# Performance work log

Measured on AMD Instinct MI355X. Metric: run time of the kernel, lower is better.

The kernel has to match this reference:

```python
import jax, jax.numpy as jnp
import numpy as np

V, F, P = 1024, 2048, 8192
_EPS = 1e-12


def setup_inputs() -> dict:
    key = jax.random.key(0)
    kv, kf, kp = jax.random.split(key, 3)
    verts = jax.random.normal(kv, (V, 3), dtype=jnp.float32)
    faces = jax.random.randint(kf, (F, 3), 0, V, dtype=jnp.int32)
    points = jax.random.normal(kp, (P, 3), dtype=jnp.float32)
    return {"verts": verts, "faces": faces, "points": points}


def _closest_point_on_tri(p, a, b, c):
    """Ericson's closest-point-on-triangle, broadcast over leading dims.
    p, a, b, c: [..., 3] -> closest point [..., 3]."""
    ab = b - a
    ac = c - a
    ap = p - a
    d1 = jnp.sum(ab * ap, -1)
    d2 = jnp.sum(ac * ap, -1)
    bp = p - b
    d3 = jnp.sum(ab * bp, -1)
    d4 = jnp.sum(ac * bp, -1)
    cp = p - c
    d5 = jnp.sum(ab * cp, -1)
    d6 = jnp.sum(ac * cp, -1)
    vc = d1 * d4 - d3 * d2
    vb = d5 * d2 - d1 * d6
    va = d3 * d6 - d5 * d4
    # guarded edge/interior parameters (denominators are >0 whenever the
    # corresponding region condition holds; eps keeps unselected branches finite)
    t_ab = d1 / jnp.maximum(d1 - d3, _EPS)
    t_ac = d2 / jnp.maximum(d2 - d6, _EPS)
    t_bc = (d4 - d3) / jnp.maximum((d4 - d3) + (d5 - d6), _EPS)
    denom = jnp.maximum(va + vb + vc, _EPS)
    v_in = vb / denom
    w_in = vc / denom
    # first-match region selection (vertex A, vertex B, edge AB, vertex C, edge AC, edge BC, interior)
    cA = (d1 <= 0) & (d2 <= 0)
    cB = (d3 >= 0) & (d4 <= d3)
    cAB = (vc <= 0) & (d1 >= 0) & (d3 <= 0)
    cC = (d6 >= 0) & (d5 <= d6)
    cAC = (vb <= 0) & (d2 >= 0) & (d6 <= 0)
    cBC = (va <= 0) & ((d4 - d3) >= 0) & ((d5 - d6) >= 0)
    z = jnp.zeros_like(d1)
    o = jnp.ones_like(d1)
    bv = jnp.select([cA, cB, cAB, cC, cAC, cBC], [z, o, t_ab, z, z, 1.0 - t_bc], v_in)
    bw = jnp.select([cA, cB, cAB, cC, cAC, cBC], [z, z, z, o, t_ac, t_bc], w_in)
    bu = 1.0 - bv - bw
    return a * bu[..., None] + b * bv[..., None] + c * bw[..., None]


def reference(verts, faces, points):
    tri = verts[faces]  # [F, 3, 3]
    a = tri[:, 0][None]  # [1, F, 3]
    b = tri[:, 1][None]
    c = tri[:, 2][None]
    cp = _closest_point_on_tri(points[:, None, :], a, b, c)  # [P, F, 3]
    dist2 = jnp.sum((points[:, None, :] - cp) ** 2, -1)  # [P, F] squared distances
    assoc = jnp.argmin(dist2, axis=1).astype(jnp.int32)  # [P] nearest triangle index
    dist = jnp.min(dist2, axis=1)  # [P]
    # loss_type == 'mse': kernel loss = sum(dist), then *= 1000 / P
    loss = jnp.sum(dist) * (1000.0 / points.shape[0])
    return loss, dist, assoc
```

## Files before the change

### kernel.cpp

```cpp
#include <hip/hip_runtime.h>

typedef float v2f __attribute__((ext_vector_type(2)));

#define P_TOTAL 8192
#define F_TOTAL 2048
#define TPB     256
#define CHUNK   256
#define NCHUNK  (F_TOTAL / CHUNK)

__device__ __forceinline__ float refine_rcp(float D) {
#pragma clang fp contract(off)
    float r0 = __builtin_amdgcn_rcpf(D);
    float e1 = __builtin_fmaf(-D, r0, 1.0f);
    return __builtin_fmaf(e1, r0, r0);
}
__device__ __forceinline__ float div_rn(float num, float D, float r) {
#pragma clang fp contract(off)
    float q0 = num * r;
    float e  = __builtin_fmaf(-D, q0, num);
    return __builtin_fmaf(e, r, q0);
}

__device__ __forceinline__ void region_select(
    float d1, float d2, float d3, float d4, float d5, float d6,
    float va, float vb, float vc, float d43, float d56,
    float g1, float g2, float g3, float g4,
    float& bu, float& bv, float& bw)
{
#pragma clang fp contract(off)
    float G1 = fmaxf(g1, 1e-12f);
    float G2 = fmaxf(g2, 1e-12f);
    float G3 = fmaxf(g3, 1e-12f);
    float G4 = fmaxf(g4, 1e-12f);

    bool cA  = (d1 <= 0.f) & (d2 <= 0.f);
    bool cB  = (d3 >= 0.f) & (d4 <= d3);
    bool cAB = (vc <= 0.f) & (d1 >= 0.f) & (d3 <= 0.f);
    bool cC  = (d6 >= 0.f) & (d5 <= d6);
    bool cAC = (vb <= 0.f) & (d2 >= 0.f) & (d6 <= 0.f);
    bool cBC = (va <= 0.f) & (d43 >= 0.f) & (d56 >= 0.f);

    float nv = cA ? 0.f : cB ? 1.f : cAB ? d1 : cC ? 0.f
             : cAC ? 0.f : cBC ? d43 : vb;
    float nw = cA ? 0.f : cB ? 0.f : cAB ? 0.f : cC ? 1.f
             : cAC ? d2 : cBC ? d43 : vc;
    float D  = cA ? 1.f : cB ? 1.f : cAB ? G1 : cC ? 1.f
             : cAC ? G2 : cBC ? G3 : G4;
    bool fBC = cBC && !(cA || cB || cAB || cC || cAC);

    float r   = refine_rcp(D);
    float qv  = div_rn(nv, D, r);
    float bww = div_rn(nw, D, r);
    float bvv = fBC ? (1.0f - qv) : qv;
    bv = bvv; bw = bww;
    bu = (1.0f - bvv) - bww;
}

__global__ __launch_bounds__(TPB) void msdf_main(
    const float* __restrict__ verts, const int* __restrict__ faces,
    const float* __restrict__ points, float* __restrict__ out)
{
#pragma clang fp contract(off)
    __shared__ float sT[9][CHUNK];
    const int tid  = threadIdx.x;
    const int lane = tid & 63;
    const int w    = tid >> 6;
    const int p    = blockIdx.x * 4 + w;

    const float px = points[3 * p], py = points[3 * p + 1], pz = points[3 * p + 2];

    unsigned int best_bits = 0xFFFFFFFFu;
    int best_idx = 0;

    for (int c = 0; c < NCHUNK; ++c) {
        __syncthreads();
        {
            int tg = c * CHUNK + tid;
            int i0 = faces[3 * tg + 0], i1 = faces[3 * tg + 1], i2 = faces[3 * tg + 2];
            sT[0][tid] = verts[3 * i0]; sT[1][tid] = verts[3 * i0 + 1]; sT[2][tid] = verts[3 * i0 + 2];
            sT[3][tid] = verts[3 * i1]; sT[4][tid] = verts[3 * i1 + 1]; sT[5][tid] = verts[3 * i1 + 2];
            sT[6][tid] = verts[3 * i2]; sT[7][tid] = verts[3 * i2 + 1]; sT[8][tid] = verts[3 * i2 + 2];
        }
        __syncthreads();

        #pragma unroll
        for (int k = 0; k < 2; ++k) {
            int base = k * 128 + 2 * lane;
            v2f ax = *(const v2f*)&sT[0][base];
            v2f ay = *(const v2f*)&sT[1][base];
            v2f az = *(const v2f*)&sT[2][base];
            v2f bx = *(const v2f*)&sT[3][base];
            v2f by = *(const v2f*)&sT[4][base];
            v2f bz = *(const v2f*)&sT[5][base];
            v2f cx = *(const v2f*)&sT[6][base];
            v2f cy = *(const v2f*)&sT[7][base];
            v2f cz = *(const v2f*)&sT[8][base];

            v2f abx = bx - ax, aby = by - ay, abz = bz - az;
            v2f acx = cx - ax, acy = cy - ay, acz = cz - az;

            v2f apx = px - ax, apy = py - ay, apz = pz - az;
            v2f d1 = (abx * apx + aby * apy) + abz * apz;
            v2f d2 = (acx * apx + acy * apy) + acz * apz;
            v2f bpx = px - bx, bpy = py - by, bpz = pz - bz;
            v2f d3 = (abx * bpx + aby * bpy) + abz * bpz;
            v2f d4 = (acx * bpx + acy * bpy) + acz * bpz;
            v2f cpx = px - cx, cpy = py - cy, cpz = pz - cz;
            v2f d5 = (abx * cpx + aby * cpy) + abz * cpz;
            v2f d6 = (acx * cpx + acy * cpy) + acz * cpz;

            v2f vc = d1 * d4 - d3 * d2;
            v2f vb = d5 * d2 - d1 * d6;
            v2f va = d3 * d6 - d5 * d4;
            v2f d43 = d4 - d3, d56 = d5 - d6;
            v2f g1 = d1 - d3;
            v2f g2 = d2 - d6;
            v2f g3 = d43 + d56;
            v2f g4 = (va + vb) + vc;

            float bu0, bv0, bw0, bu1, bv1, bw1;
            region_select(d1.x, d2.x, d3.x, d4.x, d5.x, d6.x,
                          va.x, vb.x, vc.x, d43.x, d56.x,
                          g1.x, g2.x, g3.x, g4.x, bu0, bv0, bw0);
            region_select(d1.y, d2.y, d3.y, d4.y, d5.y, d6.y,
                          va.y, vb.y, vc.y, d43.y, d56.y,
                          g1.y, g2.y, g3.y, g4.y, bu1, bv1, bw1);
            v2f bu = {bu0, bu1}, bv = {bv0, bv1}, bw = {bw0, bw1};

            v2f cpx2 = (ax * bu + bx * bv) + cx * bw;
            v2f cpy2 = (ay * bu + by * bv) + cy * bw;
            v2f cpz2 = (az * bu + bz * bv) + cz * bw;
            v2f dx = px - cpx2, dy = py - cpy2, dz = pz - cpz2;
            v2f dist2 = (dx * dx + dy * dy) + dz * dz;

            unsigned int b0 = __float_as_uint(dist2.x);
            if (b0 < best_bits) { best_bits = b0; best_idx = c * CHUNK + base; }
            unsigned int b1 = __float_as_uint(dist2.y);
            if (b1 < best_bits) { best_bits = b1; best_idx = c * CHUNK + base + 1; }
        }
    }

    unsigned long long key =
        ((unsigned long long)best_bits << 32) | (unsigned int)best_idx;
    #pragma unroll
    for (int off = 32; off > 0; off >>= 1) {
        unsigned int hi = (unsigned int)(key >> 32);
        unsigned int lo = (unsigned int)(key & 0xFFFFFFFFu);
        unsigned int ohi = __shfl_down(hi, off, 64);
        unsigned int olo = __shfl_down(lo, off, 64);
        unsigned long long ok = ((unsigned long long)ohi << 32) | olo;
        key = (ok < key) ? ok : key;
    }
    if (lane == 0) {
        out[1 + p]           = __uint_as_float((unsigned int)(key >> 32));
        out[1 + P_TOTAL + p] = (float)(unsigned int)(key & 0xFFFFFFFFu);
    }
}

__global__ __launch_bounds__(256) void msdf_loss(float* __restrict__ out)
{
    __shared__ float wsum[4];
    float s = 0.f;
    for (int k = 0; k < P_TOTAL / 256; ++k)
        s += out[1 + k * 256 + threadIdx.x];
    #pragma unroll
    for (int off = 32; off > 0; off >>= 1) s += __shfl_down(s, off, 64);
    int lane = threadIdx.x & 63, w = threadIdx.x >> 6;
    if (lane == 0) wsum[w] = s;
    __syncthreads();
    if (threadIdx.x == 0) {
        float tot = ((wsum[0] + wsum[1]) + wsum[2]) + wsum[3];
        out[0] = tot * (1000.0f / (float)P_TOTAL);
    }
}

extern "C" void kernel_launch(void* const* d_in, const int* in_sizes, int n_in,
                              void* d_out, int out_size, void* d_ws, size_t ws_size,
                              hipStream_t stream) {
    const float* verts  = (const float*)d_in[0];
    const int*   faces  = (const int*)d_in[1];
    const float* points = (const float*)d_in[2];
    float* out = (float*)d_out;

    msdf_main<<<dim3(P_TOTAL / 4), dim3(TPB), 0, stream>>>(verts, faces, points, out);
    msdf_loss<<<dim3(1), dim3(256), 0, stream>>>(out);
}
```

Before: 107.6 us.

## Double-buffer triangle staging to overlap gathers with compute

Adds a second shared-memory buffer for triangle vertices. The gather loads for the next chunk are issued into registers before computing the current chunk and written to the other buffer afterwards. This hides global-load latency behind the distance math and leaves one barrier per chunk instead of two. The cost is nine extra live registers and twice the LDS usage.

```diff
diff --git a/kernel.cpp b/kernel.cpp
--- a/kernel.cpp
+++ b/kernel.cpp
@@ -61,7 +61,7 @@
     const float* __restrict__ points, float* __restrict__ out)
 {
 #pragma clang fp contract(off)
-    __shared__ float sT[9][CHUNK];
+    __shared__ float sT[2][9][CHUNK];
     const int tid  = threadIdx.x;
     const int lane = tid & 63;
     const int w    = tid >> 6;
@@ -69,32 +69,43 @@
 
     const float px = points[3 * p], py = points[3 * p + 1], pz = points[3 * p + 2];
 
+    {
+        int tg = tid;
+        int i0 = faces[3 * tg + 0], i1 = faces[3 * tg + 1], i2 = faces[3 * tg + 2];
+        sT[0][0][tid] = verts[3 * i0]; sT[0][1][tid] = verts[3 * i0 + 1]; sT[0][2][tid] = verts[3 * i0 + 2];
+        sT[0][3][tid] = verts[3 * i1]; sT[0][4][tid] = verts[3 * i1 + 1]; sT[0][5][tid] = verts[3 * i1 + 2];
+        sT[0][6][tid] = verts[3 * i2]; sT[0][7][tid] = verts[3 * i2 + 1]; sT[0][8][tid] = verts[3 * i2 + 2];
+    }
+    __syncthreads();
+
     unsigned int best_bits = 0xFFFFFFFFu;
     int best_idx = 0;
 
     for (int c = 0; c < NCHUNK; ++c) {
-        __syncthreads();
-        {
-            int tg = c * CHUNK + tid;
+        const int cur = c & 1;
+        const bool have_next = (c + 1 < NCHUNK);
+
+        float r0, r1, r2, r3, r4, r5, r6, r7, r8;
+        if (have_next) {
+            int tg = (c + 1) * CHUNK + tid;
             int i0 = faces[3 * tg + 0], i1 = faces[3 * tg + 1], i2 = faces[3 * tg + 2];
-            sT[0][tid] = verts[3 * i0]; sT[1][tid] = verts[3 * i0 + 1]; sT[2][tid] = verts[3 * i0 + 2];
-            sT[3][tid] = verts[3 * i1]; sT[4][tid] = verts[3 * i1 + 1]; sT[5][tid] = verts[3 * i1 + 2];
-            sT[6][tid] = verts[3 * i2]; sT[7][tid] = verts[3 * i2 + 1]; sT[8][tid] = verts[3 * i2 + 2];
+            r0 = verts[3 * i0]; r1 = verts[3 * i0 + 1]; r2 = verts[3 * i0 + 2];
+            r3 = verts[3 * i1]; r4 = verts[3 * i1 + 1]; r5 = verts[3 * i1 + 2];
+            r6 = verts[3 * i2]; r7 = verts[3 * i2 + 1]; r8 = verts[3 * i2 + 2];
         }
-        __syncthreads();
 
         #pragma unroll
         for (int k = 0; k < 2; ++k) {
             int base = k * 128 + 2 * lane;
-            v2f ax = *(const v2f*)&sT[0][base];
-            v2f ay = *(const v2f*)&sT[1][base];
-            v2f az = *(const v2f*)&sT[2][base];
-            v2f bx = *(const v2f*)&sT[3][base];
-            v2f by = *(const v2f*)&sT[4][base];
-            v2f bz = *(const v2f*)&sT[5][base];
-            v2f cx = *(const v2f*)&sT[6][base];
-            v2f cy = *(const v2f*)&sT[7][base];
-            v2f cz = *(const v2f*)&sT[8][base];
+            v2f ax = *(const v2f*)&sT[cur][0][base];
+            v2f ay = *(const v2f*)&sT[cur][1][base];
+            v2f az = *(const v2f*)&sT[cur][2][base];
+            v2f bx = *(const v2f*)&sT[cur][3][base];
+            v2f by = *(const v2f*)&sT[cur][4][base];
+            v2f bz = *(const v2f*)&sT[cur][5][base];
+            v2f cx = *(const v2f*)&sT[cur][6][base];
+            v2f cy = *(const v2f*)&sT[cur][7][base];
+            v2f cz = *(const v2f*)&sT[cur][8][base];
 
             v2f abx = bx - ax, aby = by - ay, abz = bz - az;
             v2f acx = cx - ax, acy = cy - ay, acz = cz - az;
@@ -138,6 +149,14 @@
             unsigned int b1 = __float_as_uint(dist2.y);
             if (b1 < best_bits) { best_bits = b1; best_idx = c * CHUNK + base + 1; }
         }
+
+        if (have_next) {
+            int nxt = cur ^ 1;
+            sT[nxt][0][tid] = r0; sT[nxt][1][tid] = r1; sT[nxt][2][tid] = r2;
+            sT[nxt][3][tid] = r3; sT[nxt][4][tid] = r4; sT[nxt][5][tid] = r5;
+            sT[nxt][6][tid] = r6; sT[nxt][7][tid] = r7; sT[nxt][8][tid] = r8;
+        }
+        __syncthreads();
     }
 
     unsigned long long key =
```

After: 105.9 us. About the same (-1.6%).
